# Kernel optimization log

Measured on AMD Instinct MI355X. Metric: run time of the kernel, lower is better.

## Reference

```python
import jax, jax.numpy as jnp
import numpy as np

N_BLOCKS = 96
N = N_BLOCKS ** 2          # number of image blocks = n_blocks^2
D = 1024                   # feature dim (fixed by Linear(1024+1, 128))
EPS_COS = 1e-6             # eps of F.cosine_similarity
EPS_BN = 1e-5              # BatchNorm1d eps


def setup_inputs() -> dict:
    key = jax.random.key(0)
    ks = jax.random.split(key, 6)
    return {
        "features": jax.random.normal(ks[0], (N, D), dtype=jnp.float32),
        "scores": jax.random.uniform(ks[1], (N,), dtype=jnp.float32),
        "W1": jax.random.normal(ks[2], (D + 1, 128), dtype=jnp.float32) * 0.03,
        "b1": jnp.zeros((128,), jnp.float32),
        "g1": jnp.ones((128,), jnp.float32),
        "be1": jnp.zeros((128,), jnp.float32),
        "W2": jax.random.normal(ks[3], (128, 64), dtype=jnp.float32) * 0.08,
        "b2": jnp.zeros((64,), jnp.float32),
        "g2": jnp.ones((64,), jnp.float32),
        "be2": jnp.zeros((64,), jnp.float32),
        "W3": jax.random.normal(ks[4], (64, 1), dtype=jnp.float32) * 0.12,
        "b3": jnp.zeros((1,), jnp.float32),
    }


def _gaussian_similarity(features):
    # Vectorized form of the O(N^2) pairwise loop:
    #   cos_ij = <f_i, f_j> / max(|f_i||f_j|, eps)
    #   sigma^2 = D * (0.5 + 0.5 * cos)  ->  2*sigma^2 = D * (1 + cos)
    #   sim_ij = exp(-|f_i - f_j|^2 / (2*sigma^2)),  sim_ii = 1
    sq = jnp.sum(features * features, axis=-1)          # [N] squared norms
    gram = features @ features.T                          # [N, N] big GEMM
    norms = jnp.sqrt(sq)
    cos = gram / jnp.maximum(norms[:, None] * norms[None, :], EPS_COS)
    d2 = jnp.maximum(sq[:, None] + sq[None, :] - 2.0 * gram, 0.0)
    denom = jnp.maximum(jnp.float32(D) * (1.0 + cos), EPS_COS)
    sim = jnp.exp(-d2 / denom)
    eye = jnp.eye(sim.shape[0], dtype=bool)
    return jnp.where(eye, jnp.float32(1.0), sim)


def _bn_eval(h, gamma, beta):
    # BatchNorm1d in eval mode with init running stats (mean=0, var=1).
    return gamma * (h / jnp.sqrt(1.0 + EPS_BN)) + beta


def reference(features, scores, W1, b1, g1, be1, W2, b2, g2, be2, W3, b3):
    sim = _gaussian_similarity(features)                  # [N, N]
    x = jnp.concatenate([features, scores[:, None]], axis=1)  # [N, D+1]
    h = jax.nn.relu(_bn_eval(x @ W1 + b1, g1, be1))       # [N, 128]
    h = jax.nn.relu(_bn_eval(h @ W2 + b2, g2, be2))       # [N, 64]
    agg = jax.nn.sigmoid(h @ W3 + b3)[:, 0]               # [N]
    sim_mean = jnp.mean(sim, axis=1)                      # [N]
    # Torch broadcast [N,1] * [N] -> [N,N], then .mean() == mean(agg)*mean(sim_mean)
    return jnp.mean(agg) * jnp.mean(sim_mean)


if __name__ == "__main__":
    out = reference(**setup_inputs())
    print(out)
```

## Files before the change

kernel.cpp:

```cpp
#include <hip/hip_runtime.h>

#define N_IMG 9216
#define DFEAT 1024
#define NB 72

typedef __attribute__((ext_vector_type(8))) short short8;
typedef __attribute__((ext_vector_type(4))) float floatx4;
typedef __attribute__((ext_vector_type(16))) float floatx16;
typedef __attribute__((ext_vector_type(4))) int intx4;
typedef __attribute__((ext_vector_type(8))) int intx8;

__device__ __forceinline__ void async_copy16(const void* g, void* l) {
  __builtin_amdgcn_global_load_lds((const __attribute__((address_space(1))) void*)g,
                                   (__attribute__((address_space(3))) void*)l,
                                   16, 0, 0);
}

__device__ __forceinline__ unsigned short f2bf(float x) {
  union { float f; unsigned u; } a; a.f = x;
  unsigned u = a.u;
  u += 0x7fffu + ((u >> 16) & 1u);
  return (unsigned short)(u >> 16);
}

__device__ __forceinline__ intx8 ldfrag(const unsigned char* __restrict__ p) {
  intx8 v;
  *(intx4*)&v = *(const intx4*)p;
  ((intx4*)&v)[1] = *(const intx4*)(p + 16);
  return v;
}

__global__ __launch_bounds__(256) void convert_prep(const float* __restrict__ f,
                                                    const float* __restrict__ W1,
                                                    unsigned char* __restrict__ fbT,
                                                    float* __restrict__ sq,
                                                    float* __restrict__ rn,
                                                    unsigned short* __restrict__ W1t,
                                                    double* __restrict__ sums) {
  int b = blockIdx.x, t = threadIdx.x;
  if (b < 2304) {
    int lane = t & 63, wave = t >> 6;
    int row = b * 4 + wave;
    const float4* src = (const float4*)f + (size_t)row * 256;
    unsigned char* tb = fbT + (size_t)(row >> 5) * 32768 + (row & 31) * 64;
    float s = 0.f;
#pragma unroll
    for (int j = 0; j < 4; j++) {
      float4 v = src[j * 64 + lane];
      s += v.x * v.x + v.y * v.y + v.z * v.z + v.w * v.w;
      int pk = __builtin_amdgcn_cvt_pk_fp8_f32(v.x, v.y, 0, false);
      pk = __builtin_amdgcn_cvt_pk_fp8_f32(v.z, v.w, pk, true);
      int kb = j * 4 + (lane >> 4);
      *(unsigned int*)(tb + kb * 2048 + (lane & 15) * 4) = (unsigned int)pk;
    }
#pragma unroll
    for (int off = 32; off > 0; off >>= 1) s += __shfl_down(s, off, 64);
    if (lane == 0) { sq[row] = s; rn[row] = rsqrtf(s); }
  } else {
    int j = b - 2304;
    if (j == 0 && t < 2) sums[t] = 0.0;
    for (int k = t; k < DFEAT; k += 256)
      W1t[(size_t)j * DFEAT + k] = f2bf(W1[(size_t)k * 128 + j]);
  }
}

__global__ __launch_bounds__(256) void gram_sim(const unsigned char* __restrict__ fbT,
                                                const float* __restrict__ sq,
                                                const float* __restrict__ rn,
                                                double* __restrict__ sums) {
  int x = blockIdx.x & 7, i = blockIdx.x >> 3;
  int logical = (x < 4) ? (x * 329 + i) : (4 * 329 + (x - 4) * 328 + i);
  int g = 0, rem = logical;
  for (;;) { int cg = 28 + 8 * (65 - 8 * g); if (rem < cg) break; rem -= cg; g++; }
  int br, bc;
  if (rem < 28) {
    int d = 0;
    while (rem >= d + 1) { rem -= d + 1; d++; }
    bc = 8 * g + d; br = 8 * g + rem;
  } else {
    rem -= 28;
    bc = 8 * g + 7 + (rem >> 3);
    br = 8 * g + (rem & 7);
  }

  __shared__ float sqA[128], sqB[128], rnA[128], rnB[128];
  __shared__ float wpart[4];

  int t = threadIdx.x;
  int lane = t & 63, wave = t >> 6;

  if (t < 128) { sqA[t] = sq[br * 128 + t]; rnA[t] = rn[br * 128 + t]; }
  else { sqB[t - 128] = sq[bc * 128 + (t - 128)]; rnB[t - 128] = rn[bc * 128 + (t - 128)]; }
  __syncthreads();

  floatx16 acc[2][2];
#pragma unroll
  for (int a = 0; a < 2; a++)
#pragma unroll
    for (int bq = 0; bq < 2; bq++)
#pragma unroll
      for (int e = 0; e < 16; e++) acc[a][bq][e] = 0.f;

  const int wr = (wave & 1) * 64, wc = (wave >> 1) * 64;
  const int loff = (lane & 31) * 64 + (lane >> 5) * 32;

  const unsigned char* pa0 = fbT + (size_t)(br * 4 + (wr >> 5)) * 32768 + loff;
  const unsigned char* pa1 = pa0 + 32768;
  const unsigned char* pb0 = fbT + (size_t)(bc * 4 + (wc >> 5)) * 32768 + loff;
  const unsigned char* pb1 = pb0 + 32768;

#define MFMA4(A, B)                                                              \
  {                                                                              \
    acc[0][0] = __builtin_amdgcn_mfma_scale_f32_32x32x64_f8f6f4(                 \
        A[0], B[0], acc[0][0], 0, 0, 0, 0x7F7F7F7F, 0, 0x7F7F7F7F);              \
    acc[0][1] = __builtin_amdgcn_mfma_scale_f32_32x32x64_f8f6f4(                 \
        A[0], B[1], acc[0][1], 0, 0, 0, 0x7F7F7F7F, 0, 0x7F7F7F7F);              \
    acc[1][0] = __builtin_amdgcn_mfma_scale_f32_32x32x64_f8f6f4(                 \
        A[1], B[0], acc[1][0], 0, 0, 0, 0x7F7F7F7F, 0, 0x7F7F7F7F);              \
    acc[1][1] = __builtin_amdgcn_mfma_scale_f32_32x32x64_f8f6f4(                 \
        A[1], B[1], acc[1][1], 0, 0, 0, 0x7F7F7F7F, 0, 0x7F7F7F7F);              \
  }

  intx8 aC[2], bC[2], aN[2], bN[2];
  aC[0] = ldfrag(pa0); aC[1] = ldfrag(pa1);
  bC[0] = ldfrag(pb0); bC[1] = ldfrag(pb1);
#pragma unroll
  for (int kb2 = 0; kb2 < 8; kb2++) {
    const int o1 = (kb2 * 2 + 1) * 2048;
    aN[0] = ldfrag(pa0 + o1); aN[1] = ldfrag(pa1 + o1);
    bN[0] = ldfrag(pb0 + o1); bN[1] = ldfrag(pb1 + o1);
    MFMA4(aC, bC);
    if (kb2 < 7) {
      const int o2 = (kb2 * 2 + 2) * 2048;
      aC[0] = ldfrag(pa0 + o2); aC[1] = ldfrag(pa1 + o2);
      bC[0] = ldfrag(pb0 + o2); bC[1] = ldfrag(pb1 + o2);
    }
    MFMA4(aN, bN);
  }
#undef MFMA4

  const bool diag = (br == bc);
  const int r = lane & 31, kh = lane >> 5;
  (void)r;
  float lsum = 0.f;
#pragma unroll
  for (int ni = 0; ni < 2; ni++) {
    int j_loc = wc + ni * 32 + (lane & 31);
    float sj = sqB[j_loc], rnj = rnB[j_loc];
#pragma unroll
    for (int mi = 0; mi < 2; mi++) {
      int rbase = wr + mi * 32 + 4 * kh;
#pragma unroll
      for (int reg = 0; reg < 16; reg++) {
        int i_loc = rbase + (reg & 3) + 8 * (reg >> 2);
        float gv = acc[mi][ni][reg];
        float si = sqA[i_loc], rni = rnA[i_loc];
        float cosv = gv * rni * rnj;
        float den = fmaf(1024.f, cosv, 1024.f);
        float d2 = si + sj - (gv + gv);
        float arg = -d2 * __builtin_amdgcn_rcpf(den);
        float sim = __builtin_amdgcn_exp2f(arg * 1.44269504f);
        if (diag && i_loc == j_loc) sim = 1.f;
        lsum += sim;
      }
    }
  }
#pragma unroll
  for (int off = 32; off > 0; off >>= 1) lsum += __shfl_down(lsum, off, 64);
  if (lane == 0) wpart[wave] = lsum;
  __syncthreads();
  if (t == 0) {
    float tot = (wpart[0] + wpart[1] + wpart[2] + wpart[3]) * (diag ? 1.f : 2.f);
    atomicAdd(&sums[0], (double)tot);
  }
}

__global__ __launch_bounds__(256) void mlp_full(const float* __restrict__ f,
                                                const unsigned short* __restrict__ W1t,
                                                const float* __restrict__ scores,
                                                const float* __restrict__ W1,
                                                const float* __restrict__ b1,
                                                const float* __restrict__ g1,
                                                const float* __restrict__ be1,
                                                const float* __restrict__ W2, const float* __restrict__ b2,
                                                const float* __restrict__ g2, const float* __restrict__ be2,
                                                const float* __restrict__ W3, const float* __restrict__ b3,
                                                double* __restrict__ sums) {
  int r0 = blockIdx.x * 64;

  __shared__ __align__(16) float As32[64 * 32];
  __shared__ __align__(16) unsigned short Bs[128 * 32];
  __shared__ float h1s[64][128];
  __shared__ float h2s[64][65];
  __shared__ float sc[64], b1s[128], g1s[128], be1s[128], wls[128], ls[64];

  int t = threadIdx.x, lane = t & 63, wave = t >> 6;
  if (t < 64) sc[t] = scores[r0 + t];
  if (t < 128) {
    b1s[t] = b1[t]; g1s[t] = g1[t]; be1s[t] = be1[t];
    wls[t] = W1[(size_t)DFEAT * 128 + t];
  }

  floatx4 acc[2][4];
#pragma unroll
  for (int a = 0; a < 2; a++)
#pragma unroll
    for (int b = 0; b < 4; b++) acc[a][b] = (floatx4){0.f, 0.f, 0.f, 0.f};

  const int wr = (wave & 1) * 32, wc = (wave >> 1) * 64;

  for (int k0 = 0; k0 < DFEAT; k0 += 32) {
    __syncthreads();
    {
      int c = t, rA = c >> 3, p = c & 7, l = p ^ (rA & 7);
      async_copy16(f + (size_t)(r0 + rA) * DFEAT + k0 + l * 4, (char*)As32 + c * 16);
      c = t + 256; rA = c >> 3; p = c & 7; l = p ^ (rA & 7);
      async_copy16(f + (size_t)(r0 + rA) * DFEAT + k0 + l * 4, (char*)As32 + c * 16);
      c = t; int rB = c >> 2; p = c & 3; l = p ^ (rB & 3);
      async_copy16(W1t + (size_t)rB * DFEAT + k0 + l * 8, (char*)Bs + c * 16);
      c = t + 256; rB = c >> 2; p = c & 3; l = p ^ (rB & 3);
      async_copy16(W1t + (size_t)rB * DFEAT + k0 + l * 8, (char*)Bs + c * 16);
    }
    __syncthreads();

    const int mrow = lane & 15, kq = (lane >> 4) * 8;
    short8 a[2], b[4];
#pragma unroll
    for (int mt = 0; mt < 2; mt++) {
      int row = wr + mt * 16 + mrow;
      int l0 = kq >> 2;
      int p0 = l0 ^ (row & 7), p1 = (l0 + 1) ^ (row & 7);
      float4 f0 = *(const float4*)&As32[row * 32 + p0 * 4];
      float4 f1 = *(const float4*)&As32[row * 32 + p1 * 4];
      short8 af;
      af[0] = (short)f2bf(f0.x); af[1] = (short)f2bf(f0.y);
      af[2] = (short)f2bf(f0.z); af[3] = (short)f2bf(f0.w);
      af[4] = (short)f2bf(f1.x); af[5] = (short)f2bf(f1.y);
      af[6] = (short)f2bf(f1.z); af[7] = (short)f2bf(f1.w);
      a[mt] = af;
    }
#pragma unroll
    for (int nt = 0; nt < 4; nt++) {
      int row = wc + nt * 16 + mrow;
      int p = (kq >> 3) ^ (row & 3);
      b[nt] = *(const short8*)&Bs[row * 32 + p * 8];
    }
#pragma unroll
    for (int mt = 0; mt < 2; mt++)
#pragma unroll
      for (int nt = 0; nt < 4; nt++)
        acc[mt][nt] = __builtin_amdgcn_mfma_f32_16x16x32_bf16(a[mt], b[nt], acc[mt][nt], 0, 0, 0);
  }

  const float inv = 1.0f / sqrtf(1.0f + 1e-5f);
  const int rq = (lane >> 4) * 4, cn = lane & 15;
#pragma unroll
  for (int nt = 0; nt < 4; nt++) {
    int j = wc + nt * 16 + cn;
    float bj = b1s[j], gj = g1s[j] * inv, bej = be1s[j], wj = wls[j];
#pragma unroll
    for (int mt = 0; mt < 2; mt++) {
#pragma unroll
      for (int rr = 0; rr < 4; rr++) {
        int iL = wr + mt * 16 + rq + rr;
        float pre = acc[mt][nt][rr] + sc[iL] * wj + bj;
        h1s[iL][j] = fmaxf(gj * pre + bej, 0.f);
      }
    }
  }
  __syncthreads();

  {
    int j = t & 63, rg = (t >> 6) * 16;
    float a2[16];
#pragma unroll
    for (int rr = 0; rr < 16; rr++) a2[rr] = 0.f;
    for (int k = 0; k < 128; k++) {
      float w = W2[k * 64 + j];
#pragma unroll
      for (int rr = 0; rr < 16; rr++) a2[rr] = fmaf(h1s[rg + rr][k], w, a2[rr]);
    }
    float scv = g2[j] * inv, bi = b2[j], be = be2[j];
#pragma unroll
    for (int rr = 0; rr < 16; rr++)
      h2s[rg + rr][j] = fmaxf(scv * (a2[rr] + bi) + be, 0.f);
  }
  __syncthreads();

  if (t < 64) {
    float z = b3[0];
#pragma unroll
    for (int k = 0; k < 64; k++) z = fmaf(h2s[t][k], W3[k], z);
    ls[t] = 1.f / (1.f + __expf(-z));
  }
  __syncthreads();
  if (t == 0) {
    float s = 0.f;
#pragma unroll
    for (int iL = 0; iL < 64; iL++) s += ls[iL];
    atomicAdd(&sums[1], (double)s);
  }
}

__global__ void finalize(const double* __restrict__ sums, float* __restrict__ out) {
  double simmean = sums[0] / ((double)N_IMG * (double)N_IMG);
  double aggmean = sums[1] / (double)N_IMG;
  out[0] = (float)(aggmean * simmean);
}

extern "C" void kernel_launch(void* const* d_in, const int* in_sizes, int n_in,
                              void* d_out, int out_size, void* d_ws, size_t ws_size,
                              hipStream_t stream) {
  const float* f      = (const float*)d_in[0];
  const float* scores = (const float*)d_in[1];
  const float* W1 = (const float*)d_in[2];
  const float* b1 = (const float*)d_in[3];
  const float* g1 = (const float*)d_in[4];
  const float* be1 = (const float*)d_in[5];
  const float* W2 = (const float*)d_in[6];
  const float* b2 = (const float*)d_in[7];
  const float* g2 = (const float*)d_in[8];
  const float* be2 = (const float*)d_in[9];
  const float* W3 = (const float*)d_in[10];
  const float* b3 = (const float*)d_in[11];

  char* ws = (char*)d_ws;
  unsigned char* fbT  = (unsigned char*)ws;
  float* sq           = (float*)(ws + 9437184);
  float* rn           = (float*)(ws + 9474048);
  unsigned short* W1t = (unsigned short*)(ws + 9510912);
  double* sums        = (double*)(ws + 9773056);

  convert_prep<<<2432, 256, 0, stream>>>(f, W1, fbT, sq, rn, W1t, sums);
  gram_sim<<<NB * (NB + 1) / 2, 256, 0, stream>>>(fbT, sq, rn, sums);
  mlp_full<<<144, 256, 0, stream>>>(f, W1t, scores, W1, b1, g1, be1,
                                    W2, b2, g2, be2, W3, b3, sums);
  finalize<<<1, 1, 0, stream>>>(sums, (float*)d_out);
}
```

Baseline: 218.7 us.

## Stage FP8 Gram tiles through swizzled LDS with async double-buffered 128x256 tiles

The fp8 feature matrix is now stored row-major, and the gram kernel changes from 128x128 tiles read straight from global into registers to 128x256 tiles. The A and B panels are staged into double-buffered, XOR-swizzled LDS with global_load_lds async copies. Tiles are enumerated over an upper-triangular 72x36 grid, with per-element masking on the boundary tiles. The aim is to raise data reuse per loaded byte and cut redundant global traffic, at the cost of more LDS use, a barrier every k-step and extra masking work on the diagonal tiles.

```diff
diff --git a/kernel.cpp b/kernel.cpp
--- a/kernel.cpp
+++ b/kernel.cpp
@@ -2,7 +2,9 @@
 
 #define N_IMG 9216
 #define DFEAT 1024
-#define NB 72
+#define NBC 36
+#define NBR 72
+#define NPAIR 1332
 
 typedef __attribute__((ext_vector_type(8))) short short8;
 typedef __attribute__((ext_vector_type(4))) float floatx4;
@@ -23,16 +25,28 @@
   return (unsigned short)(u >> 16);
 }
 
-__device__ __forceinline__ intx8 ldfrag(const unsigned char* __restrict__ p) {
+__device__ __forceinline__ size_t sw_decode(int P) {
+  int L = P >> 3, ix = (P & 7) ^ (L & 7);
+  return (size_t)(L * 2 + (ix >> 2)) * DFEAT + (size_t)(ix & 3) * 16;
+}
+
+__device__ __forceinline__ intx4 ld16s(const unsigned char* base, int r, int c) {
+  int L = r >> 1, ix = (((r & 1) << 2) | c) ^ (L & 7);
+  return *(const intx4*)(base + L * 128 + ix * 16);
+}
+
+__device__ __forceinline__ intx8 ldfrags(const unsigned char* base, int r, int kh) {
+  intx4 lo = ld16s(base, r, kh * 2);
+  intx4 hi = ld16s(base, r, kh * 2 + 1);
   intx8 v;
-  *(intx4*)&v = *(const intx4*)p;
-  ((intx4*)&v)[1] = *(const intx4*)(p + 16);
+  v[0] = lo[0]; v[1] = lo[1]; v[2] = lo[2]; v[3] = lo[3];
+  v[4] = hi[0]; v[5] = hi[1]; v[6] = hi[2]; v[7] = hi[3];
   return v;
 }
 
 __global__ __launch_bounds__(256) void convert_prep(const float* __restrict__ f,
                                                     const float* __restrict__ W1,
-                                                    unsigned char* __restrict__ fbT,
+                                                    unsigned char* __restrict__ fb8,
                                                     float* __restrict__ sq,
                                                     float* __restrict__ rn,
                                                     unsigned short* __restrict__ W1t,
@@ -42,7 +56,7 @@
     int lane = t & 63, wave = t >> 6;
     int row = b * 4 + wave;
     const float4* src = (const float4*)f + (size_t)row * 256;
-    unsigned char* tb = fbT + (size_t)(row >> 5) * 32768 + (row & 31) * 64;
+    unsigned int* dst = (unsigned int*)(fb8 + (size_t)row * DFEAT);
     float s = 0.f;
 #pragma unroll
     for (int j = 0; j < 4; j++) {
@@ -50,8 +64,7 @@
       s += v.x * v.x + v.y * v.y + v.z * v.z + v.w * v.w;
       int pk = __builtin_amdgcn_cvt_pk_fp8_f32(v.x, v.y, 0, false);
       pk = __builtin_amdgcn_cvt_pk_fp8_f32(v.z, v.w, pk, true);
-      int kb = j * 4 + (lane >> 4);
-      *(unsigned int*)(tb + kb * 2048 + (lane & 15) * 4) = (unsigned int)pk;
+      dst[j * 64 + lane] = (unsigned int)pk;
     }
 #pragma unroll
     for (int off = 32; off > 0; off >>= 1) s += __shfl_down(s, off, 64);
@@ -64,89 +77,88 @@
   }
 }
 
-__global__ __launch_bounds__(256) void gram_sim(const unsigned char* __restrict__ fbT,
-                                                const float* __restrict__ sq,
-                                                const float* __restrict__ rn,
-                                                double* __restrict__ sums) {
-  int x = blockIdx.x & 7, i = blockIdx.x >> 3;
-  int logical = (x < 4) ? (x * 329 + i) : (4 * 329 + (x - 4) * 328 + i);
-  int g = 0, rem = logical;
-  for (;;) { int cg = 28 + 8 * (65 - 8 * g); if (rem < cg) break; rem -= cg; g++; }
-  int br, bc;
-  if (rem < 28) {
-    int d = 0;
-    while (rem >= d + 1) { rem -= d + 1; d++; }
-    bc = 8 * g + d; br = 8 * g + rem;
-  } else {
-    rem -= 28;
-    bc = 8 * g + 7 + (rem >> 3);
-    br = 8 * g + (rem & 7);
-  }
-
-  __shared__ float sqA[128], sqB[128], rnA[128], rnB[128];
+__global__ __launch_bounds__(256, 2) void gram_sim(const unsigned char* __restrict__ fb8,
+                                                   const float* __restrict__ sq,
+                                                   const float* __restrict__ rn,
+                                                   double* __restrict__ sums) {
+  int rem = blockIdx.x, bcol = 0;
+  for (;;) {
+    int m = 2 * bcol + 2; if (m > NBR) m = NBR;
+    if (rem < m) break;
+    rem -= m; bcol++;
+  }
+  int brow = rem;
+
+  __shared__ __align__(16) unsigned char Ab[2][8192];
+  __shared__ __align__(16) unsigned char Bb[2][16384];
+  __shared__ float sqA[128], rnA[128], sqB[256], rnB[256];
   __shared__ float wpart[4];
 
-  int t = threadIdx.x;
-  int lane = t & 63, wave = t >> 6;
-
-  if (t < 128) { sqA[t] = sq[br * 128 + t]; rnA[t] = rn[br * 128 + t]; }
-  else { sqB[t - 128] = sq[bc * 128 + (t - 128)]; rnB[t - 128] = rn[bc * 128 + (t - 128)]; }
-  __syncthreads();
-
-  floatx16 acc[2][2];
-#pragma unroll
-  for (int a = 0; a < 2; a++)
-#pragma unroll
-    for (int bq = 0; bq < 2; bq++)
-#pragma unroll
-      for (int e = 0; e < 16; e++) acc[a][bq][e] = 0.f;
-
-  const int wr = (wave & 1) * 64, wc = (wave >> 1) * 64;
-  const int loff = (lane & 31) * 64 + (lane >> 5) * 32;
-
-  const unsigned char* pa0 = fbT + (size_t)(br * 4 + (wr >> 5)) * 32768 + loff;
-  const unsigned char* pa1 = pa0 + 32768;
-  const unsigned char* pb0 = fbT + (size_t)(bc * 4 + (wc >> 5)) * 32768 + loff;
-  const unsigned char* pb1 = pb0 + 32768;
-
-#define MFMA4(A, B)                                                              \
-  {                                                                              \
-    acc[0][0] = __builtin_amdgcn_mfma_scale_f32_32x32x64_f8f6f4(                 \
-        A[0], B[0], acc[0][0], 0, 0, 0, 0x7F7F7F7F, 0, 0x7F7F7F7F);              \
-    acc[0][1] = __builtin_amdgcn_mfma_scale_f32_32x32x64_f8f6f4(                 \
-        A[0], B[1], acc[0][1], 0, 0, 0, 0x7F7F7F7F, 0, 0x7F7F7F7F);              \
-    acc[1][0] = __builtin_amdgcn_mfma_scale_f32_32x32x64_f8f6f4(                 \
-        A[1], B[0], acc[1][0], 0, 0, 0, 0x7F7F7F7F, 0, 0x7F7F7F7F);              \
-    acc[1][1] = __builtin_amdgcn_mfma_scale_f32_32x32x64_f8f6f4(                 \
-        A[1], B[1], acc[1][1], 0, 0, 0, 0x7F7F7F7F, 0, 0x7F7F7F7F);              \
-  }
-
-  intx8 aC[2], bC[2], aN[2], bN[2];
-  aC[0] = ldfrag(pa0); aC[1] = ldfrag(pa1);
-  bC[0] = ldfrag(pb0); bC[1] = ldfrag(pb1);
-#pragma unroll
-  for (int kb2 = 0; kb2 < 8; kb2++) {
-    const int o1 = (kb2 * 2 + 1) * 2048;
-    aN[0] = ldfrag(pa0 + o1); aN[1] = ldfrag(pa1 + o1);
-    bN[0] = ldfrag(pb0 + o1); bN[1] = ldfrag(pb1 + o1);
-    MFMA4(aC, bC);
-    if (kb2 < 7) {
-      const int o2 = (kb2 * 2 + 2) * 2048;
-      aC[0] = ldfrag(pa0 + o2); aC[1] = ldfrag(pa1 + o2);
-      bC[0] = ldfrag(pb0 + o2); bC[1] = ldfrag(pb1 + o2);
-    }
-    MFMA4(aN, bN);
-  }
-#undef MFMA4
-
-  const bool diag = (br == bc);
-  const int r = lane & 31, kh = lane >> 5;
-  (void)r;
+  int t = threadIdx.x, lane = t & 63, wave = t >> 6;
+  if (t < 128) { sqA[t] = sq[brow * 128 + t]; rnA[t] = rn[brow * 128 + t]; }
+  sqB[t] = sq[bcol * 256 + t];
+  rnB[t] = rn[bcol * 256 + t];
+
+  const unsigned char* Asrc = fb8 + (size_t)brow * 128 * DFEAT;
+  const unsigned char* Bsrc = fb8 + (size_t)bcol * 256 * DFEAT;
+
+  const size_t d0 = sw_decode(t);
+  const size_t d1 = sw_decode(t + 256);
+  const size_t d2 = sw_decode(t + 512);
+  const size_t d3 = sw_decode(t + 768);
+
+  floatx16 acc[2][4];
+#pragma unroll
+  for (int mi = 0; mi < 2; mi++)
+#pragma unroll
+    for (int ni = 0; ni < 4; ni++)
+#pragma unroll
+      for (int e = 0; e < 16; e++) acc[mi][ni][e] = 0.f;
+
+  const int wr = (wave & 1) * 64, wc = (wave >> 1) * 128;
+  const int r32 = lane & 31, kh = lane >> 5;
+
+  async_copy16(Asrc + d0, &Ab[0][t * 16]);
+  async_copy16(Asrc + d1, &Ab[0][(t + 256) * 16]);
+  async_copy16(Bsrc + d0, &Bb[0][t * 16]);
+  async_copy16(Bsrc + d1, &Bb[0][(t + 256) * 16]);
+  async_copy16(Bsrc + d2, &Bb[0][(t + 512) * 16]);
+  async_copy16(Bsrc + d3, &Bb[0][(t + 768) * 16]);
+
+  for (int kb = 0; kb < 16; kb++) {
+    __syncthreads();
+    if (kb < 15) {
+      const int nb = (kb + 1) & 1;
+      const size_t k0 = (size_t)(kb + 1) * 64;
+      async_copy16(Asrc + d0 + k0, &Ab[nb][t * 16]);
+      async_copy16(Asrc + d1 + k0, &Ab[nb][(t + 256) * 16]);
+      async_copy16(Bsrc + d0 + k0, &Bb[nb][t * 16]);
+      async_copy16(Bsrc + d1 + k0, &Bb[nb][(t + 256) * 16]);
+      async_copy16(Bsrc + d2 + k0, &Bb[nb][(t + 512) * 16]);
+      async_copy16(Bsrc + d3 + k0, &Bb[nb][(t + 768) * 16]);
+    }
+    const unsigned char* Ac = Ab[kb & 1];
+    const unsigned char* Bc = Bb[kb & 1];
+    intx8 a[2], b[4];
+#pragma unroll
+    for (int mi = 0; mi < 2; mi++) a[mi] = ldfrags(Ac, wr + mi * 32 + r32, kh);
+#pragma unroll
+    for (int ni = 0; ni < 4; ni++) b[ni] = ldfrags(Bc, wc + ni * 32 + r32, kh);
+#pragma unroll
+    for (int mi = 0; mi < 2; mi++)
+#pragma unroll
+      for (int ni = 0; ni < 4; ni++)
+        acc[mi][ni] = __builtin_amdgcn_mfma_scale_f32_32x32x64_f8f6f4(
+            a[mi], b[ni], acc[mi][ni], 0, 0, 0, 0x7F7F7F7F, 0, 0x7F7F7F7F);
+  }
+
+  const bool interior = (brow < 2 * bcol);
   float lsum = 0.f;
 #pragma unroll
-  for (int ni = 0; ni < 2; ni++) {
-    int j_loc = wc + ni * 32 + (lane & 31);
+  for (int ni = 0; ni < 4; ni++) {
+    int j_loc = wc + ni * 32 + r32;
     float sj = sqB[j_loc], rnj = rnB[j_loc];
+    int j_g = bcol * 256 + j_loc;
 #pragma unroll
     for (int mi = 0; mi < 2; mi++) {
       int rbase = wr + mi * 32 + 4 * kh;
@@ -158,21 +170,23 @@
         float cosv = gv * rni * rnj;
         float den = fmaf(1024.f, cosv, 1024.f);
         float d2 = si + sj - (gv + gv);
-        float arg = -d2 * __builtin_amdgcn_rcpf(den);
-        float sim = __builtin_amdgcn_exp2f(arg * 1.44269504f);
-        if (diag && i_loc == j_loc) sim = 1.f;
-        lsum += sim;
+        float sim = __builtin_amdgcn_exp2f(-d2 * __builtin_amdgcn_rcpf(den) * 1.44269504f);
+        if (interior) {
+          lsum += sim;
+        } else {
+          int i_g = brow * 128 + i_loc;
+          lsum += (i_g < j_g) ? 2.f * sim : (i_g == j_g ? 1.f : 0.f);
+        }
       }
     }
   }
+  if (interior) lsum *= 2.f;
 #pragma unroll
   for (int off = 32; off > 0; off >>= 1) lsum += __shfl_down(lsum, off, 64);
   if (lane == 0) wpart[wave] = lsum;
   __syncthreads();
-  if (t == 0) {
-    float tot = (wpart[0] + wpart[1] + wpart[2] + wpart[3]) * (diag ? 1.f : 2.f);
-    atomicAdd(&sums[0], (double)tot);
-  }
+  if (t == 0)
+    atomicAdd(&sums[0], (double)(wpart[0] + wpart[1] + wpart[2] + wpart[3]));
 }
 
 __global__ __launch_bounds__(256) void mlp_full(const float* __restrict__ f,
@@ -325,14 +339,14 @@
   const float* b3 = (const float*)d_in[11];
 
   char* ws = (char*)d_ws;
-  unsigned char* fbT  = (unsigned char*)ws;
+  unsigned char* fb8  = (unsigned char*)ws;
   float* sq           = (float*)(ws + 9437184);
   float* rn           = (float*)(ws + 9474048);
   unsigned short* W1t = (unsigned short*)(ws + 9510912);
   double* sums        = (double*)(ws + 9773056);
 
-  convert_prep<<<2432, 256, 0, stream>>>(f, W1, fbT, sq, rn, W1t, sums);
-  gram_sim<<<NB * (NB + 1) / 2, 256, 0, stream>>>(fbT, sq, rn, sums);
+  convert_prep<<<2432, 256, 0, stream>>>(f, W1, fb8, sq, rn, W1t, sums);
+  gram_sim<<<NPAIR, 256, 0, stream>>>(fb8, sq, rn, sums);
   mlp_full<<<144, 256, 0, stream>>>(f, W1t, scores, W1, b1, g1, be1,
                                     W2, b2, g2, be2, W3, b3, sums);
   finalize<<<1, 1, 0, stream>>>(sums, (float*)d_out);
```

After: 204.5 us. 6.5% less time.
